# Optimization experiments

Hardware: AMD Instinct MI355X
Metric: run time of the kernel (lower is better)

## Reference

```python
import jax, jax.numpy as jnp
import numpy as np

NUM_ENTITIES = 40000
NUM_RELATIONS = 500
NUM_EDGES = 400000
ENT_DIM = 50
REL_DIM = 50
NUM_HEADS = 8
UNITS = [150, 300]
NEG_SLOPE = 0.2


def setup_inputs() -> dict:
    key = jax.random.key(0)
    ks = jax.random.split(key, 12)
    h_index = jax.random.randint(ks[0], (NUM_EDGES,), 0, NUM_ENTITIES)
    r_index = jax.random.randint(ks[1], (NUM_EDGES,), 0, NUM_RELATIONS)
    t_index = jax.random.randint(ks[2], (NUM_EDGES,), 0, NUM_ENTITIES)
    std_e = np.sqrt(1.0 / ENT_DIM).astype(np.float32)
    std_r = np.sqrt(1.0 / REL_DIM).astype(np.float32)
    entity_embeddings = jax.random.truncated_normal(ks[3], -2.0, 2.0, (NUM_ENTITIES, ENT_DIM), jnp.float32) * std_e
    relation_embeddings = jax.random.truncated_normal(ks[4], -2.0, 2.0, (NUM_RELATIONS, REL_DIM), jnp.float32) * std_r
    # gat0: input ent dim 50, rel dim 50 -> concat 150, units 150
    c0 = ENT_DIM + REL_DIM + ENT_DIM
    gat0_kernel = jax.random.normal(ks[5], (NUM_HEADS, c0, UNITS[0]), jnp.float32) * (1.0 / np.sqrt(c0))
    gat0_attn = jax.random.normal(ks[6], (NUM_HEADS, UNITS[0]), jnp.float32) * (1.0 / np.sqrt(UNITS[0]))
    gat0_rel_kernel = jax.random.normal(ks[7], (REL_DIM, UNITS[0]), jnp.float32) * (1.0 / np.sqrt(REL_DIM))
    # gat1: input ent dim 8*150=1200, rel dim 150 -> concat 2550, units 300
    e1 = NUM_HEADS * UNITS[0]
    c1 = e1 + UNITS[0] + e1
    gat1_kernel = jax.random.normal(ks[8], (NUM_HEADS, c1, UNITS[1]), jnp.float32) * (1.0 / np.sqrt(c1))
    gat1_attn = jax.random.normal(ks[9], (NUM_HEADS, UNITS[1]), jnp.float32) * (1.0 / np.sqrt(UNITS[1]))
    gat1_rel_kernel = jax.random.normal(ks[10], (UNITS[0], UNITS[1]), jnp.float32) * (1.0 / np.sqrt(UNITS[0]))
    dense_w = jax.random.normal(ks[11], (ENT_DIM, UNITS[1]), jnp.float32) * (1.0 / np.sqrt(ENT_DIM))
    dense_b = jnp.zeros((UNITS[1],), jnp.float32)
    return dict(h_index=h_index, r_index=r_index, t_index=t_index,
                entity_embeddings=entity_embeddings, relation_embeddings=relation_embeddings,
                gat0_kernel=gat0_kernel, gat0_attn=gat0_attn, gat0_rel_kernel=gat0_rel_kernel,
                gat1_kernel=gat1_kernel, gat1_attn=gat1_attn, gat1_rel_kernel=gat1_rel_kernel,
                dense_w=dense_w, dense_b=dense_b)


def _kbgat_layer(h, r, t, ent, rel, kernel, attn, rel_kernel):
    """One KBGAT layer. kernel: [H, De+Dr+De, U] acting on concat(ent[h], rel[r], ent[t]).
    Split kernel so projections happen at node/relation level (equivalent, avoids E x concat_dim)."""
    N = ent.shape[0]
    De = ent.shape[1]
    Dr = rel.shape[1]
    outs = []
    for hd in range(kernel.shape[0]):
        W = kernel[hd]
        Wh, Wr, Wt = W[:De], W[De:De + Dr], W[De + Dr:]
        # message c_{hrt} = W [ent_h ; rel_r ; ent_t] : [E, U]
        c = (ent @ Wh)[h] + (rel @ Wr)[r] + (ent @ Wt)[t]
        s = jax.nn.leaky_relu(c @ attn[hd], NEG_SLOPE)  # [E]
        # segment softmax over triples sharing the same head entity
        m = jax.ops.segment_max(s, h, num_segments=N)
        e = jnp.exp(s - m[h])
        d = jax.ops.segment_sum(e, h, num_segments=N)
        a = e / (d[h] + 1e-10)
        agg = jax.ops.segment_sum(a[:, None] * c, h, num_segments=N)  # [N, U]
        outs.append(jax.nn.elu(agg))
    rel_out = rel @ rel_kernel
    return outs, rel_out


def reference(h_index, r_index, t_index, entity_embeddings, relation_embeddings,
              gat0_kernel, gat0_attn, gat0_rel_kernel,
              gat1_kernel, gat1_attn, gat1_rel_kernel, dense_w, dense_b):
    h = h_index.astype(jnp.int32)
    r = r_index.astype(jnp.int32)
    t = t_index.astype(jnp.int32)
    # dropout rate is 0.0 / inference -> identity
    outs0, rel0 = _kbgat_layer(h, r, t, entity_embeddings, relation_embeddings,
                               gat0_kernel, gat0_attn, gat0_rel_kernel)
    feat = jnp.concatenate(outs0, axis=-1)  # [N, H*U0]
    outs1, rel1 = _kbgat_layer(h, r, t, feat, rel0, gat1_kernel, gat1_attn, gat1_rel_kernel)
    ent_out = outs1[0]
    for o in outs1[1:]:
        ent_out = ent_out + o  # add_n over heads
    ent_out = ent_out + (entity_embeddings @ dense_w + dense_b)  # dense residual
    return ent_out, rel1
```

## Files before the change

kernel.cpp:

```cpp
#include <hip/hip_runtime.h>
#include <hip/hip_bf16.h>
#include <math.h>
#include <stdint.h>

typedef __attribute__((ext_vector_type(8))) __bf16 bf16x8;
typedef __attribute__((ext_vector_type(4))) float f32x4;
typedef unsigned short us;

#define GLP(p) ((__attribute__((address_space(1))) void*)(p))
#define LDP(p) ((__attribute__((address_space(3))) void*)(p))

static __device__ __forceinline__ float b2f(us u) {
    return __uint_as_float(((unsigned int)u) << 16);
}
static __device__ __forceinline__ us f2b(float f) {
    unsigned int x = __float_as_uint(f);
    return (us)((x + 0x7fffu + ((x >> 16) & 1u)) >> 16);
}

__global__ __launch_bounds__(256) void sentinel(float* out, int n, float v) {
    int i = blockIdx.x * 256 + threadIdx.x;
    if (i < n) out[i] = v;
}

__global__ __launch_bounds__(256) void zero_featpad(us* __restrict__ feat) {
    int idx = blockIdx.x * 256 + threadIdx.x;
    if (idx < 40064 * 16) {
        int n = idx >> 4, c = idx & 15;
        feat[(size_t)n * 1216 + 1200 + c] = 0;
    }
}
__global__ __launch_bounds__(256) void zero_x0pad(us* __restrict__ X0) {
    int idx = blockIdx.x * 256 + threadIdx.x;
    if (idx < 4 * 64 * 192) {
        int w = idx / (64 * 192);
        int rem = idx % (64 * 192);
        int rr = rem / 192, c = rem % 192;
        X0[((size_t)w * 40064 + 40000 + rr) * 192 + c] = 0;
    }
}

__global__ __launch_bounds__(256) void count_edges(const int* __restrict__ h, int* __restrict__ counts) {
    int e = blockIdx.x * 256 + threadIdx.x;
    if (e < 400000) atomicAdd(&counts[h[e]], 1);
}

__global__ void scan40k(const int* __restrict__ counts, int* __restrict__ rs) {
    __shared__ int part[1024];
    int tid = threadIdx.x;
    int base = tid * 40;
    int s = 0;
    for (int i = 0; i < 40; ++i) { int idx = base + i; s += (idx < 40000) ? counts[idx] : 0; }
    part[tid] = s;
    __syncthreads();
    for (int off = 1; off < 1024; off <<= 1) {
        int v = (tid >= off) ? part[tid - off] : 0;
        __syncthreads();
        part[tid] += v;
        __syncthreads();
    }
    int run = (tid == 0) ? 0 : part[tid - 1];
    for (int i = 0; i < 40; ++i) {
        int idx = base + i;
        if (idx < 40000) { rs[idx] = run; run += counts[idx]; }
    }
    if (tid == 1023) rs[40000] = part[1023];
}

__global__ __launch_bounds__(256) void scatter_edges(const int* __restrict__ h, const int* __restrict__ rs,
                                                     int* __restrict__ cursor, int* __restrict__ se) {
    int e = blockIdx.x * 256 + threadIdx.x;
    if (e < 400000) {
        int n = h[e];
        int pos = rs[n] + atomicAdd(&cursor[n], 1);
        se[pos] = e;
    }
}

__global__ __launch_bounds__(256) void pack_ent(const float* __restrict__ ent, us* __restrict__ A0) {
    int idx = blockIdx.x * 256 + threadIdx.x;
    if (idx >= 40064 * 64) return;
    int n = idx >> 6, k = idx & 63;
    A0[idx] = (n < 40000 && k < 50) ? f2b(ent[n * 50 + k]) : (us)0;
}

__global__ __launch_bounds__(256) void build_V0(const float* __restrict__ g0k, const float* __restrict__ attn0,
                                                float* __restrict__ V0) {
    int idx = blockIdx.x * 256 + threadIdx.x;
    if (idx >= 50 * 24) return;
    int k = idx / 24, g = idx % 24;
    int part = g >> 3, hd = g & 7;
    int row = k + (part == 1 ? 100 : (part == 2 ? 50 : 0));
    float s = 0.f;
    for (int u = 0; u < 150; ++u)
        s += g0k[(hd * 150 + row) * 150 + u] * attn0[hd * 150 + u];
    V0[idx] = s;
}

__global__ __launch_bounds__(256) void build_VT0(const float* __restrict__ g0k, const float* __restrict__ attn0,
                                                 us* __restrict__ VT0) {
    int idx = blockIdx.x * 256 + threadIdx.x;
    if (idx >= 128 * 64) return;
    int g = idx >> 6, k = idx & 63;
    us v = 0;
    if (g < 16 && k < 50) {
        int part = g >> 3, hd = g & 7;
        int row = part ? (100 + k) : k;
        float s = 0.f;
        for (int u = 0; u < 150; ++u)
            s += g0k[(hd * 150 + row) * 150 + u] * attn0[hd * 150 + u];
        v = f2b(s);
    }
    VT0[idx] = v;
}

__global__ __launch_bounds__(256) void build_VT1(const float* __restrict__ g1k, const float* __restrict__ attn1,
                                                 us* __restrict__ VT1) {
    int idx = blockIdx.x * 256 + threadIdx.x;
    if (idx >= 128 * 1216) return;
    int g = idx / 1216, k = idx % 1216;
    us v = 0;
    if (g < 16 && k < 1200) {
        int part = g >> 3, hd = g & 7;
        int row = part ? (1350 + k) : k;
        float s = 0.f;
        for (int u = 0; u < 300; ++u)
            s += g1k[((size_t)hd * 2550 + row) * 300 + u] * attn1[hd * 300 + u];
        v = f2b(s);
    }
    VT1[idx] = v;
}

__global__ __launch_bounds__(256) void build_Vr1(const float* __restrict__ g1k, const float* __restrict__ attn1,
                                                 float* __restrict__ Vr1) {
    int idx = blockIdx.x * 256 + threadIdx.x;
    if (idx >= 150 * 8) return;
    int k = idx / 8, hd = idx % 8;
    float s = 0.f;
    for (int u = 0; u < 300; ++u)
        s += g1k[((size_t)hd * 2550 + 1200 + k) * 300 + u] * attn1[hd * 300 + u];
    Vr1[idx] = s;
}

__global__ __launch_bounds__(256) void build_dwT(const float* __restrict__ dw, us* __restrict__ dwT) {
    int idx = blockIdx.x * 256 + threadIdx.x;
    if (idx >= 384 * 64) return;
    int j = idx >> 6, k = idx & 63;
    us v = 0;
    if (j < 300 && k < 50) v = f2b(dw[k * 300 + j]);
    dwT[idx] = v;
}

__global__ __launch_bounds__(256) void scalar_proj(const void* __restrict__ Av, int aIsF32, int lda, int K,
                                                   const float* __restrict__ V, int ldv, int col0, int G,
                                                   float* __restrict__ out) {
    __shared__ float arow[1216];
    long n = blockIdx.x;
    if (aIsF32) {
        const float* A = (const float*)Av;
        for (int k = threadIdx.x; k < K; k += 256) arow[k] = A[n * lda + k];
    } else {
        const us* A = (const us*)Av;
        for (int k = threadIdx.x; k < K; k += 256) arow[k] = b2f(A[n * lda + k]);
    }
    __syncthreads();
    int g = threadIdx.x >> 4;
    int sl = threadIdx.x & 15;
    if (g < G) {
        float s = 0.f;
        for (int k = sl; k < K; k += 16) s += arow[k] * V[k * ldv + col0 + g];
        for (int off = 8; off; off >>= 1) s += __shfl_down(s, off, 16);
        if (sl == 0) out[n * G + g] = s;
    }
}

__global__ __launch_bounds__(256) void edge_stats(const int* __restrict__ rs, const int* __restrict__ se,
                                                  const int* __restrict__ rIdx, const int* __restrict__ tIdx,
                                                  const float* __restrict__ sc, const float* __restrict__ arr,
                                                  us* __restrict__ eAT, float* __restrict__ sfac) {
    int tid = blockIdx.x * 256 + threadIdx.x;
    if (tid >= 40000 * 8) return;
    int n = tid >> 3, hd = tid & 7;
    float ah = sc[n * 16 + hd];
    int p0 = rs[n], p1 = rs[n + 1];
    float m = -INFINITY, d = 0.f;
    for (int p = p0; p < p1; ++p) {
        int e = se[p];
        float s = ah + arr[rIdx[e] * 8 + hd] + sc[tIdx[e] * 16 + 8 + hd];
        s = (s > 0.f) ? s : 0.2f * s;
        if (s > m) { d = d * expf(m - s) + 1.f; m = s; }
        else d += expf(s - m);
    }
    float inv = 1.f / (d + 1e-10f);
    us* ea = eAT + (size_t)hd * 400000;
    for (int p = p0; p < p1; ++p) {
        int e = se[p];
        float s = ah + arr[rIdx[e] * 8 + hd] + sc[tIdx[e] * 16 + 8 + hd];
        s = (s > 0.f) ? s : 0.2f * s;
        ea[p] = f2b(expf(s - m) * inv);
    }
    sfac[tid] = d * inv;
}

__global__ __launch_bounds__(256) void agg0x4(int g, const int* __restrict__ rs, const int* __restrict__ se,
                                              const int* __restrict__ rIdx, const int* __restrict__ tIdx,
                                              const us* __restrict__ eAT, const float* __restrict__ sfac,
                                              const float* __restrict__ ent, const float* __restrict__ rel,
                                              us* __restrict__ X0) {
    __shared__ int sr[128], st[128];
    __shared__ float sa[4][128];
    long n = blockIdx.x;
    int tid = threadIdx.x;
    int lane = tid & 63, wave = tid >> 6;
    int hd = 4 * g + wave;
    int k = lane;
    float ev = (k < 50) ? ent[n * 50 + k] : 0.f;
    float xh = sfac[n * 8 + hd] * ev;
    float ra = 0.f, ta = 0.f;
    int p0 = rs[n], p1 = rs[n + 1];
    for (int c0 = p0; c0 < p1; c0 += 128) {
        int cnt = min(128, p1 - c0);
        __syncthreads();
        if (tid < cnt) {
            int e = se[c0 + tid];
            sr[tid] = rIdx[e];
            st[tid] = tIdx[e];
#pragma unroll
            for (int w = 0; w < 4; ++w)
                sa[w][tid] = b2f(eAT[(size_t)(4 * g + w) * 400000 + c0 + tid]);
        }
        __syncthreads();
#pragma unroll 4
        for (int i = 0; i < cnt; ++i) {
            float a = sa[wave][i];
            int r = sr[i], t = st[i];
            if (k < 50) {
                ra += a * rel[r * 50 + k];
                ta += a * ent[(long)t * 50 + k];
            }
        }
    }
    us* row = X0 + ((size_t)wave * 40064 + n) * 192;
    if (k < 50) { row[k] = f2b(xh); row[50 + k] = f2b(ra); row[100 + k] = f2b(ta); }
    if (lane < 42) row[150 + lane] = 0;
}

__global__ __launch_bounds__(256) void build_B0T8(const float* __restrict__ g0k, us* __restrict__ B) {
    int idx = blockIdx.x * 256 + threadIdx.x;
    if (idx >= 8 * 256 * 192) return;
    int hd = idx / (256 * 192);
    int u = (idx / 192) % 256, k = idx % 192;
    us v = 0;
    if (u < 150 && k < 150) v = f2b(g0k[((size_t)hd * 150 + k) * 150 + u]);
    B[idx] = v;
}

__global__ __launch_bounds__(256) void build_B1Th2(int g, const float* __restrict__ g1k, us* __restrict__ B) {
    int idx = blockIdx.x * 256 + threadIdx.x;
    if (idx >= 1280 * 1216) return;
    int j = idx / 1216, k = idx % 1216;
    us v = 0;
    if (j < 1216 && k < 1200) {
        int blk = j / 304, u = j % 304;
        if (u < 300) {
            int hd = 2 * g + (blk & 1);
            int row = (blk >= 2) ? (1350 + k) : k;
            v = f2b(g1k[((size_t)hd * 2550 + row) * 300 + u]);
        }
    }
    B[idx] = v;
}

#define GEMM_BODY(EPILOG)                                                                       \
    __shared__ __align__(16) us As[2][128 * 64];                                                \
    __shared__ __align__(16) us Bs[2][128 * 64];                                                \
    const int tid = threadIdx.x;                                                                \
    const int lane = tid & 63, wave = tid >> 6;                                                 \
    const int wr = wave >> 1, wc = wave & 1;                                                    \
    const int r16 = lane & 15, g4 = lane >> 4;                                                  \
    const int gx = gridDim.x;                                                                   \
    const int nwg = gx * gridDim.y;                                                             \
    const int orig = blockIdx.y * gx + blockIdx.x;                                              \
    const int q8 = nwg >> 3, r8 = nwg & 7;                                                      \
    const int xcd = orig & 7;                                                                   \
    const int lg = (xcd < r8 ? xcd * (q8 + 1) : r8 * (q8 + 1) + (xcd - r8) * q8) + (orig >> 3); \
    const long bm = lg / gx, bn = lg % gx;                                                      \
    f32x4 acc[4][4];                                                                            \
    _Pragma("unroll") for (int m = 0; m < 4; ++m)                                               \
        _Pragma("unroll") for (int n = 0; n < 4; ++n) acc[m][n] = (f32x4){0.f, 0.f, 0.f, 0.f};  \
    auto stage = [&](int buf, int kt) {                                                         \
        _Pragma("unroll") for (int i = 0; i < 4; ++i) {                                         \
            int idx = tid + i * 256;                                                            \
            int row = idx >> 3, sub = idx & 7;                                                  \
            int scol = ((sub ^ (row & 7)) << 3);                                                \
            const us* ga = A + (bm * 128 + row) * (long)K + kt + scol;                          \
            __builtin_amdgcn_global_load_lds(GLP(ga), LDP(&As[buf][idx * 8]), 16, 0, 0);        \
        }                                                                                       \
        _Pragma("unroll") for (int i = 0; i < 4; ++i) {                                         \
            int idx = tid + i * 256;                                                            \
            int row = idx >> 3, sub = idx & 7;                                                  \
            int scol = ((sub ^ (row & 7)) << 3);                                                \
            const us* gb = BT + (bn * 128 + row) * (long)K + kt + scol;                         \
            __builtin_amdgcn_global_load_lds(GLP(gb), LDP(&Bs[buf][idx * 8]), 16, 0, 0);        \
        }                                                                                       \
    };                                                                                          \
    const int nt = K >> 6;                                                                      \
    stage(0, 0);                                                                                \
    const int sxor = (r16 & 7) << 3;                                                            \
    for (int t = 0; t < nt; ++t) {                                                              \
        int cur = t & 1;                                                                        \
        if (t + 1 < nt) {                                                                       \
            stage(cur ^ 1, (t + 1) << 6);                                                       \
            asm volatile("s_waitcnt vmcnt(8)" ::: "memory");                                    \
        } else {                                                                                \
            asm volatile("s_waitcnt vmcnt(0)" ::: "memory");                                    \
        }                                                                                       \
        __builtin_amdgcn_s_barrier();                                                           \
        asm volatile("" ::: "memory");                                                          \
        __builtin_amdgcn_s_setprio(1);                                                          \
        _Pragma("unroll") for (int kk = 0; kk < 2; ++kk) {                                      \
            bf16x8 af[4], bfr[4];                                                               \
            _Pragma("unroll") for (int m = 0; m < 4; ++m)                                       \
                af[m] = *(const bf16x8*)&As[cur][(wr * 64 + m * 16 + r16) * 64 +                \
                                               ((kk * 32 + g4 * 8) ^ sxor)];                    \
            _Pragma("unroll") for (int n = 0; n < 4; ++n)                                       \
                bfr[n] = *(const bf16x8*)&Bs[cur][(wc * 64 + n * 16 + r16) * 64 +               \
                                                ((kk * 32 + g4 * 8) ^ sxor)];                   \
            _Pragma("unroll") for (int m = 0; m < 4; ++m)                                       \
                _Pragma("unroll") for (int n = 0; n < 4; ++n)                                   \
                    acc[m][n] = __builtin_amdgcn_mfma_f32_16x16x32_bf16(af[m], bfr[n],          \
                                                                        acc[m][n], 0, 0, 0);    \
        }                                                                                       \
        __builtin_amdgcn_s_setprio(0);                                                          \
        asm volatile("" ::: "memory");                                                          \
        __builtin_amdgcn_s_barrier();                                                           \
    }                                                                                           \
    _Pragma("unroll") for (int m = 0; m < 4; ++m)                                               \
        _Pragma("unroll") for (int n = 0; n < 4; ++n)                                           \
            _Pragma("unroll") for (int j = 0; j < 4; ++j) { EPILOG }

__global__ __launch_bounds__(256) void gemm_bt(const us* __restrict__ A_, const us* __restrict__ BT_,
                                               us* __restrict__ C, int K, int ldc, int nColReal,
                                               int colOff0, int colOffZ, long aStrideZ, long btStrideZ,
                                               int act) {
    const int z = blockIdx.z;
    const us* A = A_ + (size_t)z * aStrideZ;
    const us* BT = BT_ + (size_t)z * btStrideZ;
    const int colBase = colOff0 + z * colOffZ;
    GEMM_BODY(
        int cc = (int)bn * 128 + wc * 64 + n * 16 + r16;
        if (cc < nColReal) {
            long row = bm * 128 + wr * 64 + m * 16 + g4 * 4 + j;
            float v = acc[m][n][j];
            if (act) v = (v > 0.f) ? v : expm1f(v);
            C[row * (long)ldc + colBase + cc] = f2b(v);
        })
}

__global__ __launch_bounds__(256) void gemm_bt_f32(const us* __restrict__ A, const us* __restrict__ BT,
                                                   float* __restrict__ C, int K, int ldc, int nColReal,
                                                   const float* __restrict__ bias) {
    GEMM_BODY(
        int cc = (int)bn * 128 + wc * 64 + n * 16 + r16;
        if (cc < nColReal) {
            long row = bm * 128 + wr * 64 + m * 16 + g4 * 4 + j;
            float v = acc[m][n][j];
            if (bias) v += bias[cc];
            C[row * (long)ldc + cc] = v;
        })
}

__global__ __launch_bounds__(256) void rel0_kernel(const float* __restrict__ rel, const float* __restrict__ g0rk,
                                                   float* __restrict__ rel0b) {
    int idx = blockIdx.x * 256 + threadIdx.x;
    if (idx >= 500 * 150) return;
    int rI = idx / 150, u = idx % 150;
    float s = 0.f;
    for (int k = 0; k < 50; ++k) s += rel[rI * 50 + k] * g0rk[k * 150 + u];
    rel0b[idx] = s;
}

__global__ __launch_bounds__(256) void pr1_kernel(const float* __restrict__ rel0b, const float* __restrict__ g1k,
                                                  us* __restrict__ PR1b) {
    int idx = blockIdx.x * 256 + threadIdx.x;
    if (idx >= 500 * 2400) return;
    int rI = idx / 2400, jj = idx % 2400;
    int hd = jj / 300, u = jj % 300;
    float s = 0.f;
    for (int k = 0; k < 150; ++k)
        s += rel0b[rI * 150 + k] * g1k[((size_t)hd * 2550 + 1200 + k) * 300 + u];
    PR1b[idx] = f2b(s);
}

__global__ __launch_bounds__(256) void rel1_kernel(const float* __restrict__ rel0b, const float* __restrict__ g1rk,
                                                   float* __restrict__ out) {
    int idx = blockIdx.x * 256 + threadIdx.x;
    if (idx >= 500 * 300) return;
    int rI = idx / 300, u = idx % 300;
    float s = 0.f;
    for (int k = 0; k < 150; ++k) s += rel0b[rI * 150 + k] * g1rk[k * 300 + u];
    out[idx] = s;
}

__global__ __launch_bounds__(256) void agg1h2(int g, const int* __restrict__ rs, const int* __restrict__ se,
                                              const int* __restrict__ rIdx, const int* __restrict__ tIdx,
                                              const us* __restrict__ eAT, const float* __restrict__ sfac,
                                              const us* __restrict__ C1g2, const us* __restrict__ PR1b,
                                              float* __restrict__ outf) {
    __shared__ int sr[128], st[128];
    __shared__ float sa0[128], sa1[128];
    long n = blockIdx.x;
    int tid = threadIdx.x;
    int hd0 = 2 * g, hd1 = hd0 + 1;
    int d = tid, d2 = tid + 256;
    bool a2 = (d2 < 300);
    float sf0 = sfac[n * 8 + hd0], sf1 = sfac[n * 8 + hd1];
    const us* crow = C1g2 + (size_t)n * 1216;
    float acc00 = sf0 * b2f(crow[d]);
    float acc10 = sf1 * b2f(crow[304 + d]);
    float acc01 = a2 ? sf0 * b2f(crow[d2]) : 0.f;
    float acc11 = a2 ? sf1 * b2f(crow[304 + d2]) : 0.f;
    const us* ea0 = eAT + (size_t)hd0 * 400000;
    const us* ea1 = eAT + (size_t)hd1 * 400000;
    int p0 = rs[n], p1 = rs[n + 1];
    for (int c0 = p0; c0 < p1; c0 += 128) {
        int cnt = min(128, p1 - c0);
        __syncthreads();
        if (tid < cnt) {
            int e = se[c0 + tid];
            sr[tid] = rIdx[e];
            st[tid] = tIdx[e];
            sa0[tid] = b2f(ea0[c0 + tid]);
            sa1[tid] = b2f(ea1[c0 + tid]);
        }
        __syncthreads();
#pragma unroll 4
        for (int i = 0; i < cnt; ++i) {
            int r = sr[i], t = st[i];
            float a0 = sa0[i], a1 = sa1[i];
            const us* ct = C1g2 + (size_t)t * 1216;
            const us* pr = PR1b + (size_t)r * 2400;
            acc00 += a0 * (b2f(pr[hd0 * 300 + d]) + b2f(ct[608 + d]));
            acc10 += a1 * (b2f(pr[hd1 * 300 + d]) + b2f(ct[912 + d]));
            if (a2) {
                acc01 += a0 * (b2f(pr[hd0 * 300 + d2]) + b2f(ct[608 + d2]));
                acc11 += a1 * (b2f(pr[hd1 * 300 + d2]) + b2f(ct[912 + d2]));
            }
        }
    }
    float v00 = (acc00 > 0.f) ? acc00 : expm1f(acc00);
    float v10 = (acc10 > 0.f) ? acc10 : expm1f(acc10);
    outf[n * 300 + d] += v00 + v10;
    if (a2) {
        float v01 = (acc01 > 0.f) ? acc01 : expm1f(acc01);
        float v11 = (acc11 > 0.f) ? acc11 : expm1f(acc11);
        outf[n * 300 + d2] += v01 + v11;
    }
}

extern "C" void kernel_launch(void* const* d_in, const int* in_sizes, int n_in,
                              void* d_out, int out_size, void* d_ws, size_t ws_size,
                              hipStream_t stream) {
    const int* hIdx = (const int*)d_in[0];
    const int* rIdx = (const int*)d_in[1];
    const int* tIdx = (const int*)d_in[2];
    const float* ent  = (const float*)d_in[3];
    const float* rel  = (const float*)d_in[4];
    const float* g0k  = (const float*)d_in[5];
    const float* at0w = (const float*)d_in[6];
    const float* g0rk = (const float*)d_in[7];
    const float* g1k  = (const float*)d_in[8];
    const float* at1w = (const float*)d_in[9];
    const float* g1rk = (const float*)d_in[10];
    const float* dw   = (const float*)d_in[11];
    const float* db   = (const float*)d_in[12];
    float* outf = (float*)d_out;

    {
        const int exp_sz[13] = {400000, 400000, 400000, 2000000, 25000, 180000, 1200,
                                7500, 6120000, 2400, 45000, 15000, 300};
        bool ok = (n_in == 13);
        for (int i = 0; ok && i < 13; ++i) ok = (in_sizes[i] == exp_sz[i]);
        if (!ok) {
            sentinel<<<(out_size + 255) / 256, 256, 0, stream>>>(outf, out_size, 44.0f);
            return;
        }
    }

    char* p = (char*)d_ws;
    auto carve = [&](size_t bytes) -> char* {
        char* r = p;
        p += (bytes + 255) & ~(size_t)255;
        return r;
    };
    int* counts = (int*)carve(40000 * 4);
    int* cursor = (int*)carve(40000 * 4);
    int* rs     = (int*)carve(40001 * 4);
    int* se     = (int*)carve(400000 * 4);
    float* sc   = (float*)carve((size_t)40064 * 16 * 4);
    float* arS  = (float*)carve(500 * 8 * 4);
    us* eAT     = (us*)carve((size_t)8 * 400000 * 2);
    float* sfac = (float*)carve((size_t)40000 * 8 * 4);
    float* V0  = (float*)carve(50 * 24 * 4);
    float* Vr1 = (float*)carve(150 * 8 * 4);
    float* rel0b = (float*)carve(500 * 150 * 4);
    us* PR1b  = (us*)carve((size_t)500 * 2400 * 2);
    us* VT0   = (us*)carve((size_t)128 * 64 * 2);
    us* VT1   = (us*)carve((size_t)128 * 1216 * 2);
    us* dwT   = (us*)carve((size_t)384 * 64 * 2);
    us* B0T8  = (us*)carve((size_t)8 * 256 * 192 * 2);
    us* B1Th2 = (us*)carve((size_t)1280 * 1216 * 2);
    us* feat  = (us*)carve((size_t)40064 * 1216 * 2);
    char* tail = p;
    us* A0   = (us*)tail;
    us* X0   = (us*)tail;
    us* C1g2 = (us*)tail;
    size_t tailNeed = (size_t)40064 * 1216 * 2;
    size_t totalNeed = (size_t)(tail - (char*)d_ws) + tailNeed;
    if (totalNeed > ws_size) {
        sentinel<<<(out_size + 255) / 256, 256, 0, stream>>>(outf, out_size, 42.0f);
        return;
    }

    hipMemsetAsync(counts, 0, 40000 * 4, stream);
    hipMemsetAsync(cursor, 0, 40000 * 4, stream);
    zero_featpad<<<(40064 * 16 + 255) / 256, 256, 0, stream>>>(feat);

    count_edges<<<1563, 256, 0, stream>>>(hIdx, counts);
    scan40k<<<1, 1024, 0, stream>>>(counts, rs);
    scatter_edges<<<1563, 256, 0, stream>>>(hIdx, rs, cursor, se);

    pack_ent<<<(40064 * 64 + 255) / 256, 256, 0, stream>>>(ent, A0);
    build_VT0<<<(128 * 64 + 255) / 256, 256, 0, stream>>>(g0k, at0w, VT0);
    gemm_bt_f32<<<dim3(1, 313), 256, 0, stream>>>(A0, VT0, sc, 64, 16, 16, nullptr);
    build_dwT<<<(384 * 64 + 255) / 256, 256, 0, stream>>>(dw, dwT);
    gemm_bt_f32<<<dim3(3, 313), 256, 0, stream>>>(A0, dwT, outf, 64, 300, 300, db);
    build_V0<<<5, 256, 0, stream>>>(g0k, at0w, V0);
    scalar_proj<<<500, 256, 0, stream>>>(rel, 1, 50, 50, V0, 24, 16, 8, arS);
    edge_stats<<<1250, 256, 0, stream>>>(rs, se, rIdx, tIdx, sc, arS, eAT, sfac);

    zero_x0pad<<<(4 * 64 * 192 + 255) / 256, 256, 0, stream>>>(X0);
    build_B0T8<<<(8 * 256 * 192 + 255) / 256, 256, 0, stream>>>(g0k, B0T8);
    for (int g = 0; g < 2; ++g) {
        agg0x4<<<40000, 256, 0, stream>>>(g, rs, se, rIdx, tIdx, eAT, sfac, ent, rel, X0);
        gemm_bt<<<dim3(2, 313, 4), 256, 0, stream>>>(X0, B0T8 + (size_t)g * 4 * 256 * 192, feat,
                                                     192, 1216, 150, g * 600, 150,
                                                     (long)40064 * 192, (long)256 * 192, 1);
    }

    rel0_kernel<<<(500 * 150 + 255) / 256, 256, 0, stream>>>(rel, g0rk, rel0b);
    build_VT1<<<(128 * 1216 + 255) / 256, 256, 0, stream>>>(g1k, at1w, VT1);
    build_Vr1<<<5, 256, 0, stream>>>(g1k, at1w, Vr1);
    gemm_bt_f32<<<dim3(1, 313), 256, 0, stream>>>(feat, VT1, sc, 1216, 16, 16, nullptr);
    scalar_proj<<<500, 256, 0, stream>>>(rel0b, 1, 150, 150, Vr1, 8, 0, 8, arS);
    edge_stats<<<1250, 256, 0, stream>>>(rs, se, rIdx, tIdx, sc, arS, eAT, sfac);
    pr1_kernel<<<(500 * 2400 + 255) / 256, 256, 0, stream>>>(rel0b, g1k, PR1b);

    for (int g = 0; g < 4; ++g) {
        build_B1Th2<<<(1280 * 1216 + 255) / 256, 256, 0, stream>>>(g, g1k, B1Th2);
        gemm_bt<<<dim3(10, 313, 1), 256, 0, stream>>>(feat, B1Th2, C1g2,
                                                      1216, 1216, 1216, 0, 0, 0, 0, 0);
        agg1h2<<<40000, 256, 0, stream>>>(g, rs, se, rIdx, tIdx, eAT, sfac, C1g2, PR1b, outf);
    }

    rel1_kernel<<<(500 * 300 + 255) / 256, 256, 0, stream>>>(rel0b, g1rk, outf + (size_t)40000 * 300);
}
```

Before: 1.968 ms.

## Single-buffer GEMM LDS, tile-transpose B1 build, cache edge scores in edge_stats

The bf16 GEMM body drops its double-buffered LDS staging and uses a single 32KB A/B tile pair with full waits and barriers each k-step. This halves LDS per block, which may allow more resident blocks per CU, but it removes the overlap of global loads with MFMA work. build_B1Th2 becomes a 64x64 LDS tile transpose so reads from g1k along u are coalesced. edge_stats now writes leaky-ReLU scores to a scratch buffer in the first pass and reads them back in the second, so the index and score gathers are not repeated.

```diff
diff --git a/kernel.cpp b/kernel.cpp
--- a/kernel.cpp
+++ b/kernel.cpp
@@ -174,10 +174,11 @@
     }
 }
 
-__global__ __launch_bounds__(256) void edge_stats(const int* __restrict__ rs, const int* __restrict__ se,
-                                                  const int* __restrict__ rIdx, const int* __restrict__ tIdx,
-                                                  const float* __restrict__ sc, const float* __restrict__ arr,
-                                                  us* __restrict__ eAT, float* __restrict__ sfac) {
+__global__ __launch_bounds__(256) void edge_stats2(const int* __restrict__ rs, const int* __restrict__ se,
+                                                   const int* __restrict__ rIdx, const int* __restrict__ tIdx,
+                                                   const float* __restrict__ sc, const float* __restrict__ arr,
+                                                   us* __restrict__ eAT, float* __restrict__ sfac,
+                                                   float* __restrict__ sS) {
     int tid = blockIdx.x * 256 + threadIdx.x;
     if (tid >= 40000 * 8) return;
     int n = tid >> 3, hd = tid & 7;
@@ -188,15 +189,14 @@
         int e = se[p];
         float s = ah + arr[rIdx[e] * 8 + hd] + sc[tIdx[e] * 16 + 8 + hd];
         s = (s > 0.f) ? s : 0.2f * s;
+        sS[(size_t)p * 8 + hd] = s;
         if (s > m) { d = d * expf(m - s) + 1.f; m = s; }
         else d += expf(s - m);
     }
     float inv = 1.f / (d + 1e-10f);
     us* ea = eAT + (size_t)hd * 400000;
     for (int p = p0; p < p1; ++p) {
-        int e = se[p];
-        float s = ah + arr[rIdx[e] * 8 + hd] + sc[tIdx[e] * 16 + 8 + hd];
-        s = (s > 0.f) ? s : 0.2f * s;
+        float s = sS[(size_t)p * 8 + hd];
         ea[p] = f2b(expf(s - m) * inv);
     }
     sfac[tid] = d * inv;
@@ -255,25 +255,37 @@
     B[idx] = v;
 }
 
-__global__ __launch_bounds__(256) void build_B1Th2(int g, const float* __restrict__ g1k, us* __restrict__ B) {
-    int idx = blockIdx.x * 256 + threadIdx.x;
-    if (idx >= 1280 * 1216) return;
-    int j = idx / 1216, k = idx % 1216;
-    us v = 0;
-    if (j < 1216 && k < 1200) {
-        int blk = j / 304, u = j % 304;
-        if (u < 300) {
-            int hd = 2 * g + (blk & 1);
-            int row = (blk >= 2) ? (1350 + k) : k;
-            v = f2b(g1k[((size_t)hd * 2550 + row) * 300 + u]);
+__global__ __launch_bounds__(256) void build_B1Th2T(int g, const float* __restrict__ g1k, us* __restrict__ B) {
+    __shared__ us tile[64][65];
+    int j0 = blockIdx.x * 64, k0 = blockIdx.y * 64;
+    int tl = threadIdx.x & 63, th = threadIdx.x >> 6;
+#pragma unroll 4
+    for (int i = 0; i < 16; ++i) {
+        int jj = j0 + tl;
+        int kk = k0 + th + 4 * i;
+        us v = 0;
+        if (jj < 1216 && kk < 1200) {
+            int blk = jj / 304, u = jj % 304;
+            if (u < 300) {
+                int hd = 2 * g + (blk & 1);
+                int row = (blk >= 2) ? (1350 + kk) : kk;
+                v = f2b(g1k[((size_t)hd * 2550 + row) * 300 + u]);
+            }
         }
-    }
-    B[idx] = v;
+        tile[tl][th + 4 * i] = v;
+    }
+    __syncthreads();
+#pragma unroll 4
+    for (int i = 0; i < 16; ++i) {
+        int k = k0 + tl;
+        int j = j0 + th + 4 * i;
+        if (j < 1280 && k < 1216) B[(size_t)j * 1216 + k] = tile[th + 4 * i][tl];
+    }
 }
 
 #define GEMM_BODY(EPILOG)                                                                       \
-    __shared__ __align__(16) us As[2][128 * 64];                                                \
-    __shared__ __align__(16) us Bs[2][128 * 64];                                                \
+    __shared__ __align__(16) us As[128 * 64];                                                   \
+    __shared__ __align__(16) us Bs[128 * 64];                                                   \
     const int tid = threadIdx.x;                                                                \
     const int lane = tid & 63, wave = tid >> 6;                                                 \
     const int wr = wave >> 1, wc = wave & 1;                                                    \
@@ -288,52 +300,42 @@
     f32x4 acc[4][4];                                                                            \
     _Pragma("unroll") for (int m = 0; m < 4; ++m)                                               \
         _Pragma("unroll") for (int n = 0; n < 4; ++n) acc[m][n] = (f32x4){0.f, 0.f, 0.f, 0.f};  \
-    auto stage = [&](int buf, int kt) {                                                         \
+    const int nt = K >> 6;                                                                      \
+    const int sxor = (r16 & 7) << 3;                                                            \
+    for (int t = 0; t < nt; ++t) {                                                              \
+        int kt = t << 6;                                                                        \
         _Pragma("unroll") for (int i = 0; i < 4; ++i) {                                         \
             int idx = tid + i * 256;                                                            \
             int row = idx >> 3, sub = idx & 7;                                                  \
             int scol = ((sub ^ (row & 7)) << 3);                                                \
             const us* ga = A + (bm * 128 + row) * (long)K + kt + scol;                          \
-            __builtin_amdgcn_global_load_lds(GLP(ga), LDP(&As[buf][idx * 8]), 16, 0, 0);        \
+            __builtin_amdgcn_global_load_lds(GLP(ga), LDP(&As[idx * 8]), 16, 0, 0);             \
         }                                                                                       \
         _Pragma("unroll") for (int i = 0; i < 4; ++i) {                                         \
             int idx = tid + i * 256;                                                            \
             int row = idx >> 3, sub = idx & 7;                                                  \
             int scol = ((sub ^ (row & 7)) << 3);                                                \
             const us* gb = BT + (bn * 128 + row) * (long)K + kt + scol;                         \
-            __builtin_amdgcn_global_load_lds(GLP(gb), LDP(&Bs[buf][idx * 8]), 16, 0, 0);        \
+            __builtin_amdgcn_global_load_lds(GLP(gb), LDP(&Bs[idx * 8]), 16, 0, 0);             \
         }                                                                                       \
-    };                                                                                          \
-    const int nt = K >> 6;                                                                      \
-    stage(0, 0);                                                                                \
-    const int sxor = (r16 & 7) << 3;                                                            \
-    for (int t = 0; t < nt; ++t) {                                                              \
-        int cur = t & 1;                                                                        \
-        if (t + 1 < nt) {                                                                       \
-            stage(cur ^ 1, (t + 1) << 6);                                                       \
-            asm volatile("s_waitcnt vmcnt(8)" ::: "memory");                                    \
-        } else {                                                                                \
-            asm volatile("s_waitcnt vmcnt(0)" ::: "memory");                                    \
-        }                                                                                       \
-        __builtin_amdgcn_s_barrier();                                                           \
-        asm volatile("" ::: "memory");                                                          \
+        asm volatile("s_waitcnt vmcnt(0)" ::: "memory");                                        \
+        __syncthreads();                                                                        \
         __builtin_amdgcn_s_setprio(1);                                                          \
         _Pragma("unroll") for (int kk = 0; kk < 2; ++kk) {                                      \
             bf16x8 af[4], bfr[4];                                                               \
             _Pragma("unroll") for (int m = 0; m < 4; ++m)                                       \
-                af[m] = *(const bf16x8*)&As[cur][(wr * 64 + m * 16 + r16) * 64 +                \
-                                               ((kk * 32 + g4 * 8) ^ sxor)];                    \
+                af[m] = *(const bf16x8*)&As[(wr * 64 + m * 16 + r16) * 64 +                     \
+                                            ((kk * 32 + g4 * 8) ^ sxor)];                       \
             _Pragma("unroll") for (int n = 0; n < 4; ++n)                                       \
-                bfr[n] = *(const bf16x8*)&Bs[cur][(wc * 64 + n * 16 + r16) * 64 +               \
-                                                ((kk * 32 + g4 * 8) ^ sxor)];                   \
+                bfr[n] = *(const bf16x8*)&Bs[(wc * 64 + n * 16 + r16) * 64 +                    \
+                                             ((kk * 32 + g4 * 8) ^ sxor)];                      \
             _Pragma("unroll") for (int m = 0; m < 4; ++m)                                       \
                 _Pragma("unroll") for (int n = 0; n < 4; ++n)                                   \
                     acc[m][n] = __builtin_amdgcn_mfma_f32_16x16x32_bf16(af[m], bfr[n],          \
                                                                         acc[m][n], 0, 0, 0);    \
         }                                                                                       \
         __builtin_amdgcn_s_setprio(0);                                                          \
-        asm volatile("" ::: "memory");                                                          \
-        __builtin_amdgcn_s_barrier();                                                           \
+        __syncthreads();                                                                        \
     }                                                                                           \
     _Pragma("unroll") for (int m = 0; m < 4; ++m)                                               \
         _Pragma("unroll") for (int n = 0; n < 4; ++n)                                           \
@@ -512,9 +514,10 @@
     us* B1Th2 = (us*)carve((size_t)1280 * 1216 * 2);
     us* feat  = (us*)carve((size_t)40064 * 1216 * 2);
     char* tail = p;
-    us* A0   = (us*)tail;
-    us* X0   = (us*)tail;
-    us* C1g2 = (us*)tail;
+    us* A0    = (us*)tail;
+    float* sS = (float*)tail;
+    us* X0    = (us*)tail;
+    us* C1g2  = (us*)tail;
     size_t tailNeed = (size_t)40064 * 1216 * 2;
     size_t totalNeed = (size_t)(tail - (char*)d_ws) + tailNeed;
     if (totalNeed > ws_size) {
@@ -537,7 +540,7 @@
     gemm_bt_f32<<<dim3(3, 313), 256, 0, stream>>>(A0, dwT, outf, 64, 300, 300, db);
     build_V0<<<5, 256, 0, stream>>>(g0k, at0w, V0);
     scalar_proj<<<500, 256, 0, stream>>>(rel, 1, 50, 50, V0, 24, 16, 8, arS);
-    edge_stats<<<1250, 256, 0, stream>>>(rs, se, rIdx, tIdx, sc, arS, eAT, sfac);
+    edge_stats2<<<1250, 256, 0, stream>>>(rs, se, rIdx, tIdx, sc, arS, eAT, sfac, sS);
 
     zero_x0pad<<<(4 * 64 * 192 + 255) / 256, 256, 0, stream>>>(X0);
     build_B0T8<<<(8 * 256 * 192 + 255) / 256, 256, 0, stream>>>(g0k, B0T8);
@@ -553,11 +556,11 @@
     build_Vr1<<<5, 256, 0, stream>>>(g1k, at1w, Vr1);
     gemm_bt_f32<<<dim3(1, 313), 256, 0, stream>>>(feat, VT1, sc, 1216, 16, 16, nullptr);
     scalar_proj<<<500, 256, 0, stream>>>(rel0b, 1, 150, 150, Vr1, 8, 0, 8, arS);
-    edge_stats<<<1250, 256, 0, stream>>>(rs, se, rIdx, tIdx, sc, arS, eAT, sfac);
+    edge_stats2<<<1250, 256, 0, stream>>>(rs, se, rIdx, tIdx, sc, arS, eAT, sfac, sS);
     pr1_kernel<<<(500 * 2400 + 255) / 256, 256, 0, stream>>>(rel0b, g1k, PR1b);
 
     for (int g = 0; g < 4; ++g) {
-        build_B1Th2<<<(1280 * 1216 + 255) / 256, 256, 0, stream>>>(g, g1k, B1Th2);
+        build_B1Th2T<<<dim3(20, 19), 256, 0, stream>>>(g, g1k, B1Th2);
         gemm_bt<<<dim3(10, 313, 1), 256, 0, stream>>>(feat, B1Th2, C1g2,
                                                       1216, 1216, 1216, 0, 0, 0, 0, 0);
         agg1h2<<<40000, 256, 0, stream>>>(g, rs, se, rIdx, tIdx, eAT, sfac, C1g2, PR1b, outf);
```

New measurement: 2.077 ms. +5.5%, slower.
